# Performance work log

Hardware: AMD Instinct MI355X
Metric: run time of the kernel (lower is better)

The kernel has to match this reference:

```python
import jax, jax.numpy as jnp
import numpy as np

EPS = 1e-6
ALPHA = 0.2  # LeakyReLU negative slope


def layer_norm(x, g, b):
    mu = jnp.mean(x, axis=-1, keepdims=True)
    var = jnp.mean(jnp.square(x - mu), axis=-1, keepdims=True)
    return (x - mu) * jax.lax.rsqrt(var + EPS) * g + b


def graph_attention(x, bias, W, a_src, a_dst):
    # x: [B,N,D], bias: [B,N,N], W: [D, H*Dh], a_src/a_dst: [H, Dh]
    B, N, D = x.shape
    H, Dh = a_src.shape
    h = jnp.einsum('bnd,dhk->bhnk', x, W.reshape(D, H, Dh))  # [B,H,N,Dh]
    s = jnp.einsum('bhnk,hk->bhn', h, a_src)                 # source term
    t = jnp.einsum('bhnk,hk->bhn', h, a_dst)                 # target term
    e = jax.nn.leaky_relu(s[:, :, :, None] + t[:, :, None, :], ALPHA)
    e = e + bias[:, None, :, :]                              # graph mask/bias
    attn = jax.nn.softmax(e, axis=-1)                        # [B,H,N,N]
    out = jnp.einsum('bhij,bhjk->bhik', attn, h)             # [B,H,N,Dh]
    return out.transpose(0, 2, 1, 3).reshape(B, N, H * Dh)


def setup_inputs() -> dict:
    key = jax.random.key(0)
    ks = jax.random.split(key, 8)
    B, N, D, H = 2, 2048, 512, 8
    Dh = D // H
    sc = 1.0 / np.sqrt(D)
    return {
        'x': jax.random.normal(ks[0], (B, N, D), jnp.float32),
        'bias': jax.random.normal(ks[1], (B, N, N), jnp.float32),
        'W1': jax.random.normal(ks[2], (D, D), jnp.float32) * sc,
        'a_src1': jax.random.normal(ks[3], (H, Dh), jnp.float32) * sc,
        'a_dst1': jax.random.normal(ks[4], (H, Dh), jnp.float32) * sc,
        'g1': jnp.ones((D,), jnp.float32),
        'b1': jnp.zeros((D,), jnp.float32),
        'W2': jax.random.normal(ks[5], (D, D), jnp.float32) * sc,
        'a_src2': jax.random.normal(ks[6], (1, D), jnp.float32) * sc,
        'a_dst2': jax.random.normal(ks[7], (1, D), jnp.float32) * sc,
        'g2': jnp.ones((D,), jnp.float32),
        'b2': jnp.zeros((D,), jnp.float32),
    }


def reference(x, bias, W1, a_src1, a_dst1, g1, b1, W2, a_src2, a_dst2, g2, b2):
    # dropout is identity in eval mode
    attn_in = layer_norm(x, g1, b1)
    attn = graph_attention(attn_in, bias, W1, a_src1, a_dst1) + x
    attn_in2 = layer_norm(attn, g2, b2)
    out = graph_attention(attn_in2, bias, W2, a_src2, a_dst2) + attn
    return out
```

## Files before the change

kernel.cpp:

```cpp
#include <hip/hip_runtime.h>
#include <math.h>

#define NB 2
#define NN 2048
#define DD 512

typedef __attribute__((ext_vector_type(8))) short short8;
typedef __attribute__((ext_vector_type(4))) float f32x4;

__device__ __forceinline__ unsigned short f2bf(float x) {
  union { float f; unsigned u; } a;
  a.f = x;
  unsigned r = a.u + 0x7FFF + ((a.u >> 16) & 1);
  return (unsigned short)(r >> 16);
}
__device__ __forceinline__ float bf2f(unsigned short u) {
  union { unsigned u; float f; } a;
  a.u = ((unsigned)u) << 16;
  return a.f;
}
__device__ __forceinline__ unsigned cvtpk(float lo, float hi) {
  unsigned r;
  asm("v_cvt_pk_bf16_f32 %0, %1, %2" : "=v"(r) : "v"(lo), "v"(hi));
  return r;
}

__device__ __forceinline__ float waveReduceSum(float v) {
#pragma unroll
  for (int o = 32; o; o >>= 1) v += __shfl_down(v, o, 64);
  return v;
}
__device__ __forceinline__ float blockReduceSum(float v, float* red4) {
  int tid = threadIdx.x;
  __syncthreads();
  v = waveReduceSum(v);
  if ((tid & 63) == 0) red4[tid >> 6] = v;
  __syncthreads();
  return red4[0] + red4[1] + red4[2] + red4[3];
}

__global__ __launch_bounds__(256) void ln_kernel(const float* __restrict__ x,
                                                 const float* __restrict__ g,
                                                 const float* __restrict__ bb,
                                                 unsigned short* __restrict__ y) {
  int row = blockIdx.x;
  int t = threadIdx.x;
  const float* xr = x + (size_t)row * DD;
  __shared__ float red4[4];
  float2 v = *(const float2*)&xr[2 * t];
  float s = blockReduceSum(v.x + v.y, red4);
  float mu = s * (1.0f / 512.0f);
  float d0 = v.x - mu, d1 = v.y - mu;
  float ss = blockReduceSum(d0 * d0 + d1 * d1, red4);
  float rstd = rsqrtf(ss * (1.0f / 512.0f) + 1e-6f);
  float2 gg = *(const float2*)&g[2 * t];
  float2 bv = *(const float2*)&bb[2 * t];
  ushort2 o;
  o.x = f2bf(d0 * rstd * gg.x + bv.x);
  o.y = f2bf(d1 * rstd * gg.y + bv.y);
  *(ushort2*)&y[(size_t)row * DD + 2 * t] = o;
}

__global__ __launch_bounds__(256) void wt2_kernel(const float* __restrict__ W1,
                                                  const float* __restrict__ W2,
                                                  unsigned short* __restrict__ WT1,
                                                  unsigned short* __restrict__ WT2) {
  const float* W = blockIdx.z ? W2 : W1;
  unsigned short* WT = blockIdx.z ? WT2 : WT1;
  __shared__ float tile[64][65];
  int kt = blockIdx.x * 64, ct = blockIdx.y * 64;
  int t = threadIdx.x;
#pragma unroll
  for (int u = 0; u < 16; u++) {
    int lin = t + u * 256;
    int kl = lin >> 6, cl = lin & 63;
    tile[kl][cl] = W[(size_t)(kt + kl) * DD + ct + cl];
  }
  __syncthreads();
#pragma unroll
  for (int u = 0; u < 16; u++) {
    int lin = t + u * 256;
    int cl = lin >> 6, kl = lin & 63;
    WT[(size_t)(ct + cl) * DD + kt + kl] = f2bf(tile[kl][cl]);
  }
}

__global__ __launch_bounds__(256) void v2_kernel(
    const float* __restrict__ W1, const float* __restrict__ as1,
    const float* __restrict__ ad1, float* __restrict__ vs1, float* __restrict__ vd1,
    const float* __restrict__ W2, const float* __restrict__ as2,
    const float* __restrict__ ad2, float* __restrict__ vs2, float* __restrict__ vd2) {
  int slot = blockIdx.y;
  const float *W, *as, *ad;
  float *vs, *vd;
  int Dh, hoff;
  if (slot < 8) {
    W = W1; as = as1 + slot * 64; ad = ad1 + slot * 64;
    vs = vs1 + (size_t)slot * DD; vd = vd1 + (size_t)slot * DD;
    Dh = 64; hoff = slot * 64;
  } else {
    W = W2; as = as2; ad = ad2; vs = vs2; vd = vd2;
    Dh = 512; hoff = 0;
  }
  int t = threadIdx.x;
  int dl = t >> 2, kq = t & 3;
  int d = blockIdx.x * 64 + dl;
  int kn = Dh >> 2;
  const float* wr = W + (size_t)d * DD + hoff + kq * kn;
  const float* asp = as + kq * kn;
  const float* adp = ad + kq * kn;
  float s = 0.f, dd2 = 0.f;
  for (int k = 0; k < kn; k++) {
    float wv = wr[k];
    s += wv * asp[k];
    dd2 += wv * adp[k];
  }
  s += __shfl_xor(s, 1);
  s += __shfl_xor(s, 2);
  dd2 += __shfl_xor(dd2, 1);
  dd2 += __shfl_xor(dd2, 2);
  if (kq == 0) {
    vs[d] = s;
    vd[d] = dd2;
  }
}

__global__ __launch_bounds__(256) void biasH_kernel(const float* __restrict__ bias,
                                                    unsigned short* __restrict__ biasH) {
  int row = blockIdx.x;
  int t = threadIdx.x;
  const float* br = bias + (size_t)row * NN;
  float4 a = *(const float4*)&br[t * 4];
  float4 c = *(const float4*)&br[t * 4 + 1024];
  uint2 d0, d1;
  d0.x = cvtpk(a.x, a.y);
  d0.y = cvtpk(a.z, a.w);
  d1.x = cvtpk(c.x, c.y);
  d1.y = cvtpk(c.z, c.w);
  *(uint2*)&biasH[(size_t)row * NN + t * 4] = d0;
  *(uint2*)&biasH[(size_t)row * NN + t * 4 + 1024] = d1;
}

__global__ __launch_bounds__(256) void gemm_kernel(const unsigned short* __restrict__ A,
                                                   const unsigned short* __restrict__ BT,
                                                   unsigned short* __restrict__ hbT) {
  __shared__ float accL[4][16][65];
  int t = threadIdx.x, w = t >> 6, l = t & 63;
  int li = l & 15, lg = l >> 4;
  int R0 = blockIdx.x * 16;
  int c0 = blockIdx.y * 64;
  const unsigned short* ar = A + (size_t)(R0 + li) * DD + w * 128 + lg * 8;
  const unsigned short* br = BT + (size_t)(c0 + li) * DD + w * 128 + lg * 8;
  f32x4 acc[4] = {};
#pragma unroll
  for (int k0 = 0; k0 < 128; k0 += 32) {
    short8 af = *(const short8*)(ar + k0);
#pragma unroll
    for (int f = 0; f < 4; f++) {
      short8 bf = *(const short8*)(br + (size_t)f * 16 * DD + k0);
      acc[f] = __builtin_amdgcn_mfma_f32_16x16x32_bf16(af, bf, acc[f], 0, 0, 0);
    }
  }
#pragma unroll
  for (int f = 0; f < 4; f++)
#pragma unroll
    for (int r = 0; r < 4; r++) accL[w][lg * 4 + r][f * 16 + li] = acc[f][r];
  __syncthreads();
  int b = R0 >> 11, jT = (R0 & (NN - 1)) >> 4;
  int cT0 = c0 >> 4;
#pragma unroll
  for (int u = 0; u < 2; u++) {
    int idx = t + u * 256;
    int f = idx >> 7;
    int rem = idx & 127;
    int cl = rem >> 3, jlp = rem & 7;
    int cc = f * 16 + cl;
    float v0 = accL[0][2 * jlp][cc] + accL[1][2 * jlp][cc] + accL[2][2 * jlp][cc] +
               accL[3][2 * jlp][cc];
    float v1 = accL[0][2 * jlp + 1][cc] + accL[1][2 * jlp + 1][cc] +
               accL[2][2 * jlp + 1][cc] + accL[3][2 * jlp + 1][cc];
    size_t off = (((size_t)(b * (DD / 16) + cT0 + f) * (NN / 16)) + jT) * 256 +
                 cl * 16 + jlp * 2;
    *(unsigned*)(hbT + off) = cvtpk(v0, v1);
  }
}

__global__ __launch_bounds__(256) void st_kernel(const unsigned short* __restrict__ lnB,
                                                 const float* __restrict__ vs,
                                                 const float* __restrict__ vd,
                                                 float* __restrict__ sOut,
                                                 float* __restrict__ tOut, int HN) {
  int t = threadIdx.x, w = t >> 6, l = t & 63;
  int row = blockIdx.x * 4 + w;
  int b = row >> 11, n = row & (NN - 1);
  const unsigned short* lr = lnB + (size_t)row * DD + l * 8;
  union { short8 v; unsigned short u[8]; } xv;
  xv.v = *(const short8*)lr;
  float xf[8];
#pragma unroll
  for (int k = 0; k < 8; k++) xf[k] = bf2f(xv.u[k]);
  for (int h = 0; h < HN; h++) {
    const float* vsr = vs + (size_t)h * DD + l * 8;
    const float* vdr = vd + (size_t)h * DD + l * 8;
    float4 a0 = *(const float4*)vsr, a1 = *(const float4*)(vsr + 4);
    float4 c0 = *(const float4*)vdr, c1 = *(const float4*)(vdr + 4);
    float ps = xf[0] * a0.x + xf[1] * a0.y + xf[2] * a0.z + xf[3] * a0.w +
               xf[4] * a1.x + xf[5] * a1.y + xf[6] * a1.z + xf[7] * a1.w;
    float pd = xf[0] * c0.x + xf[1] * c0.y + xf[2] * c0.z + xf[3] * c0.w +
               xf[4] * c1.x + xf[5] * c1.y + xf[6] * c1.z + xf[7] * c1.w;
#pragma unroll
    for (int o = 32; o; o >>= 1) {
      ps += __shfl_xor(ps, o);
      pd += __shfl_xor(pd, o);
    }
    if (l == 0) {
      sOut[((size_t)b * HN + h) * NN + n] = ps;
      tOut[((size_t)b * HN + h) * NN + n] = pd;
    }
  }
}

template <int HN, int CCH>
__global__ __launch_bounds__(256) void pv_kernel(
    const unsigned short* __restrict__ hbT, const unsigned short* __restrict__ biasH,
    const float* __restrict__ sArr, const float* __restrict__ tArr,
    const float* __restrict__ res, float* __restrict__ out) {
  constexpr int DH = DD / HN;
  __shared__ unsigned short Pl[4][512];
  __shared__ float accL[4][16][33];
  __shared__ float sL[4][16];
  int t = threadIdx.x, w = t >> 6, l = t & 63;
  int li = l & 15, lg = l >> 4;
  int i0 = blockIdx.x * 16;
  int ck = blockIdx.y, bh = blockIdx.z;
  int h = bh % HN, b = bh / HN;
  int c0 = h * DH + ck * (CCH * 64);
  size_t bhN = (size_t)bh * NN;
  const float* trow = tArr + bhN;

  int rs = l >> 3;
  int js = (l & 7) * 4;
  int wq = (((l & 7) >> 1) ^ (rs & 3)) * 8 + (l & 1) * 4;
  float sv[2];
  sv[0] = sArr[bhN + i0 + rs];
  sv[1] = sArr[bhN + i0 + 8 + rs];
  const unsigned short* bbH = biasH + ((size_t)b * NN + i0) * NN;

  const unsigned short* vb =
      hbT + (((size_t)(b * (DD / 16) + (c0 >> 4)) * (NN / 16) + (lg >> 1)) * 256) +
      li * 16 + (lg & 1) * 8;
  int ra0 = li * 32 + ((lg ^ (li & 3)) * 8);

  const int jbeg = w * (NN / 4), jend = jbeg + NN / 4;
  f32x4 acc[CCH][4] = {};
  float psum[2] = {0.f, 0.f};

  float4 ptv = *(const float4*)&trow[jbeg + js];
  uint2 pb0 = *(const uint2*)&bbH[(size_t)(0 * 8 + rs) * NN + jbeg + js];
  uint2 pb1 = *(const uint2*)&bbH[(size_t)(1 * 8 + rs) * NN + jbeg + js];
  short8 nv[CCH][4];
#pragma unroll
  for (int cc = 0; cc < CCH; cc++)
#pragma unroll
    for (int f = 0; f < 4; f++)
      nv[cc][f] = *(const short8*)(vb + (size_t)jbeg * 16 + (size_t)(cc * 4 + f) * 32768);

  for (int jt = jbeg; jt < jend; jt += 32) {
    float4 tv = ptv;
    uint2 bq0 = pb0, bq1 = pb1;
    short8 v[CCH][4];
#pragma unroll
    for (int cc = 0; cc < CCH; cc++)
#pragma unroll
      for (int f = 0; f < 4; f++) v[cc][f] = nv[cc][f];
    if (jt + 32 < jend) {
      int jb = jt + 32 + js;
      ptv = *(const float4*)&trow[jb];
      pb0 = *(const uint2*)&bbH[(size_t)(0 * 8 + rs) * NN + jb];
      pb1 = *(const uint2*)&bbH[(size_t)(1 * 8 + rs) * NN + jb];
#pragma unroll
      for (int cc = 0; cc < CCH; cc++)
#pragma unroll
        for (int f = 0; f < 4; f++)
          nv[cc][f] = *(const short8*)(vb + (size_t)(jt + 32) * 16 +
                                       (size_t)(cc * 4 + f) * 32768);
    }
#pragma unroll
    for (int u = 0; u < 2; u++) {
      union { uint2 v; unsigned short q[4]; } bu;
      bu.v = u ? bq1 : bq0;
      int row = u * 8 + rs;
      float e0 = sv[u] + tv.x;
      float e1 = sv[u] + tv.y;
      float e2 = sv[u] + tv.z;
      float e3 = sv[u] + tv.w;
      e0 = fmaxf(e0, 0.2f * e0) + bf2f(bu.q[0]);
      e1 = fmaxf(e1, 0.2f * e1) + bf2f(bu.q[1]);
      e2 = fmaxf(e2, 0.2f * e2) + bf2f(bu.q[2]);
      e3 = fmaxf(e3, 0.2f * e3) + bf2f(bu.q[3]);
      float p0 = __expf(e0);
      float p1 = __expf(e1);
      float p2 = __expf(e2);
      float p3 = __expf(e3);
      psum[u] += (p0 + p1) + (p2 + p3);
      uint2 d;
      d.x = cvtpk(p0, p1);
      d.y = cvtpk(p2, p3);
      *(uint2*)&Pl[w][row * 32 + wq] = d;
    }
    short8 a0 = *(const short8*)&Pl[w][ra0];
    __builtin_amdgcn_s_setprio(1);
#pragma unroll
    for (int cc = 0; cc < CCH; cc++)
#pragma unroll
      for (int f = 0; f < 4; f++)
        acc[cc][f] = __builtin_amdgcn_mfma_f32_16x16x32_bf16(a0, v[cc][f], acc[cc][f], 0, 0, 0);
    __builtin_amdgcn_s_setprio(0);
  }
#pragma unroll
  for (int u = 0; u < 2; u++) {
    float r = psum[u];
    r += __shfl_xor(r, 1);
    r += __shfl_xor(r, 2);
    r += __shfl_xor(r, 4);
    if ((l & 7) == 0) sL[w][u * 8 + rs] = r;
  }
#pragma unroll
  for (int g = 0; g < 2 * CCH; g++) {
    int cc = g >> 1, half = g & 1;
#pragma unroll
    for (int f = 0; f < 2; f++)
#pragma unroll
      for (int r = 0; r < 4; r++)
        accL[w][lg * 4 + r][f * 16 + li] = acc[cc][half * 2 + f][r];
    __syncthreads();
    {
      int rr = t >> 4, cp = (t & 15) * 2;
      float S = sL[0][rr] + sL[1][rr] + sL[2][rr] + sL[3][rr];
      float inv = 1.0f / S;
      float2 O = {0.f, 0.f};
#pragma unroll
      for (int w2 = 0; w2 < 4; w2++) {
        O.x += accL[w2][rr][cp];
        O.y += accL[w2][rr][cp + 1];
      }
      size_t ix = ((size_t)b * NN + i0 + rr) * DD + c0 + cc * 64 + half * 32 + cp;
      float2 rv = *(const float2*)&res[ix];
      float2 ov = {O.x * inv + rv.x, O.y * inv + rv.y};
      *(float2*)&out[ix] = ov;
    }
    __syncthreads();
  }
}

extern "C" void kernel_launch(void* const* d_in, const int* in_sizes, int n_in,
                              void* d_out, int out_size, void* d_ws, size_t ws_size,
                              hipStream_t stream) {
  const float* x = (const float*)d_in[0];
  const float* bias = (const float*)d_in[1];
  const float* W1 = (const float*)d_in[2];
  const float* asrc1 = (const float*)d_in[3];
  const float* adst1 = (const float*)d_in[4];
  const float* g1 = (const float*)d_in[5];
  const float* b1 = (const float*)d_in[6];
  const float* W2 = (const float*)d_in[7];
  const float* asrc2 = (const float*)d_in[8];
  const float* adst2 = (const float*)d_in[9];
  const float* g2 = (const float*)d_in[10];
  const float* b2 = (const float*)d_in[11];
  float* out = (float*)d_out;
  float* ws = (float*)d_ws;

  const size_t RC = (size_t)NB * NN * DD;
  float* attnBuf = ws;
  unsigned short* lnB = (unsigned short*)(ws + RC);
  unsigned short* hbT = (unsigned short*)(ws + RC + RC / 2);
  unsigned short* WT1 = (unsigned short*)(ws + 2 * RC);
  unsigned short* WT2 = WT1 + (size_t)DD * DD;
  float* vs1 = (float*)(WT2 + (size_t)DD * DD);
  float* vd1 = vs1 + 8 * DD;
  float* vs2 = vd1 + 8 * DD;
  float* vd2 = vs2 + DD;
  float* sBuf = vd2 + DD;
  float* tBuf = sBuf + 16 * NN;
  unsigned short* biasH = (unsigned short*)(tBuf + 16 * NN);

  const int rows = NB * NN;

  hipLaunchKernelGGL(wt2_kernel, dim3(8, 8, 2), dim3(256), 0, stream, W1, W2, WT1, WT2);
  hipLaunchKernelGGL(v2_kernel, dim3(8, 9), dim3(256), 0, stream, W1, asrc1, adst1, vs1, vd1,
                     W2, asrc2, adst2, vs2, vd2);
  hipLaunchKernelGGL(biasH_kernel, dim3(rows), dim3(256), 0, stream, bias, biasH);

  hipLaunchKernelGGL(ln_kernel, dim3(rows), dim3(256), 0, stream, x, g1, b1, lnB);
  hipLaunchKernelGGL(gemm_kernel, dim3(256, 8), dim3(256), 0, stream, lnB, WT1, hbT);
  hipLaunchKernelGGL(st_kernel, dim3(rows / 4), dim3(256), 0, stream, lnB, vs1, vd1, sBuf, tBuf, 8);
  hipLaunchKernelGGL((pv_kernel<8, 1>), dim3(128, 1, 16), dim3(256), 0, stream, hbT, biasH,
                     sBuf, tBuf, x, attnBuf);

  hipLaunchKernelGGL(ln_kernel, dim3(rows), dim3(256), 0, stream, attnBuf, g2, b2, lnB);
  hipLaunchKernelGGL(gemm_kernel, dim3(256, 8), dim3(256), 0, stream, lnB, WT2, hbT);
  hipLaunchKernelGGL(st_kernel, dim3(rows / 4), dim3(256), 0, stream, lnB, vs2, vd2, sBuf, tBuf, 1);
  hipLaunchKernelGGL((pv_kernel<1, 2>), dim3(128, 4, 2), dim3(256), 0, stream, hbT, biasH,
                     sBuf, tBuf, attnBuf, out);
}
```

Before: 170.5 us.

## Retile transposed V layout into 64-column blocks and compute softmax row sums via MFMA

The projection kernel now writes the transposed bf16 h in 64-column blocks, so the four 16-column fragments a PV block reads for one key tile sit next to each other rather than 32K elements apart. This is meant to improve locality and DRAM page behaviour on the V loads. The PV kernel also drops the per-lane fp32 running sums and shuffle reduction, and computes the softmax denominator with one extra MFMA against a vector of bf16 ones. The denominator is therefore summed from bf16-rounded probabilities, which matches the numerator but costs one more MFMA per tile.

New measurement: 167.2 us. About the same (-1.9%).

```diff
diff --git a/kernel.cpp b/kernel.cpp
--- a/kernel.cpp
+++ b/kernel.cpp
@@ -167,7 +167,6 @@
     for (int r = 0; r < 4; r++) accL[w][lg * 4 + r][f * 16 + li] = acc[f][r];
   __syncthreads();
   int b = R0 >> 11, jT = (R0 & (NN - 1)) >> 4;
-  int cT0 = c0 >> 4;
 #pragma unroll
   for (int u = 0; u < 2; u++) {
     int idx = t + u * 256;
@@ -179,8 +178,8 @@
                accL[3][2 * jlp][cc];
     float v1 = accL[0][2 * jlp + 1][cc] + accL[1][2 * jlp + 1][cc] +
                accL[2][2 * jlp + 1][cc] + accL[3][2 * jlp + 1][cc];
-    size_t off = (((size_t)(b * (DD / 16) + cT0 + f) * (NN / 16)) + jT) * 256 +
-                 cl * 16 + jlp * 2;
+    size_t off = (((size_t)(b * (DD / 64) + blockIdx.y) * (NN / 16)) + jT) * 1024 +
+                 f * 256 + cl * 16 + jlp * 2;
     *(unsigned*)(hbT + off) = cvtpk(v0, v1);
   }
 }
@@ -228,7 +227,7 @@
   constexpr int DH = DD / HN;
   __shared__ unsigned short Pl[4][512];
   __shared__ float accL[4][16][33];
-  __shared__ float sL[4][16];
+  __shared__ float sLa[4][16];
   int t = threadIdx.x, w = t >> 6, l = t & 63;
   int li = l & 15, lg = l >> 4;
   int i0 = blockIdx.x * 16;
@@ -244,30 +243,36 @@
   float sv[2];
   sv[0] = sArr[bhN + i0 + rs];
   sv[1] = sArr[bhN + i0 + 8 + rs];
-  const unsigned short* bbH = biasH + ((size_t)b * NN + i0) * NN;
-
-  const unsigned short* vb =
-      hbT + (((size_t)(b * (DD / 16) + (c0 >> 4)) * (NN / 16) + (lg >> 1)) * 256) +
-      li * 16 + (lg & 1) * 8;
+  const unsigned short* bb0 = biasH + ((size_t)b * NN + i0 + rs) * NN;
+  const unsigned short* bb1 = bb0 + (size_t)8 * NN;
+
+  const unsigned short* vbase =
+      hbT + ((size_t)(b * (DD / 64) + (c0 >> 6)) * (NN / 16)) * 1024 +
+      (lg >> 1) * 1024 + li * 16 + (lg & 1) * 8;
   int ra0 = li * 32 + ((lg ^ (li & 3)) * 8);
+
+  union { short8 v; unsigned short q[8]; } ones;
+#pragma unroll
+  for (int k = 0; k < 8; k++) ones.q[k] = 0x3F80;
 
   const int jbeg = w * (NN / 4), jend = jbeg + NN / 4;
   f32x4 acc[CCH][4] = {};
-  float psum[2] = {0.f, 0.f};
+  f32x4 accS = {0.f, 0.f, 0.f, 0.f};
 
   float4 ptv = *(const float4*)&trow[jbeg + js];
-  uint2 pb0 = *(const uint2*)&bbH[(size_t)(0 * 8 + rs) * NN + jbeg + js];
-  uint2 pb1 = *(const uint2*)&bbH[(size_t)(1 * 8 + rs) * NN + jbeg + js];
+  uint2 pq0 = *(const uint2*)&bb0[jbeg + js];
+  uint2 pq1 = *(const uint2*)&bb1[jbeg + js];
   short8 nv[CCH][4];
 #pragma unroll
-  for (int cc = 0; cc < CCH; cc++)
-#pragma unroll
-    for (int f = 0; f < 4; f++)
-      nv[cc][f] = *(const short8*)(vb + (size_t)jbeg * 16 + (size_t)(cc * 4 + f) * 32768);
+  for (int cc = 0; cc < CCH; cc++) {
+    const unsigned short* vp = vbase + (size_t)cc * ((NN / 16) * 1024) + (size_t)jbeg * 64;
+#pragma unroll
+    for (int f = 0; f < 4; f++) nv[cc][f] = *(const short8*)(vp + f * 256);
+  }
 
   for (int jt = jbeg; jt < jend; jt += 32) {
     float4 tv = ptv;
-    uint2 bq0 = pb0, bq1 = pb1;
+    uint2 bq0 = pq0, bq1 = pq1;
     short8 v[CCH][4];
 #pragma unroll
     for (int cc = 0; cc < CCH; cc++)
@@ -276,14 +281,15 @@
     if (jt + 32 < jend) {
       int jb = jt + 32 + js;
       ptv = *(const float4*)&trow[jb];
-      pb0 = *(const uint2*)&bbH[(size_t)(0 * 8 + rs) * NN + jb];
-      pb1 = *(const uint2*)&bbH[(size_t)(1 * 8 + rs) * NN + jb];
-#pragma unroll
-      for (int cc = 0; cc < CCH; cc++)
-#pragma unroll
-        for (int f = 0; f < 4; f++)
-          nv[cc][f] = *(const short8*)(vb + (size_t)(jt + 32) * 16 +
-                                       (size_t)(cc * 4 + f) * 32768);
+      pq0 = *(const uint2*)&bb0[jb];
+      pq1 = *(const uint2*)&bb1[jb];
+#pragma unroll
+      for (int cc = 0; cc < CCH; cc++) {
+        const unsigned short* vp =
+            vbase + (size_t)cc * ((NN / 16) * 1024) + (size_t)(jt + 32) * 64;
+#pragma unroll
+        for (int f = 0; f < 4; f++) nv[cc][f] = *(const short8*)(vp + f * 256);
+      }
     }
 #pragma unroll
     for (int u = 0; u < 2; u++) {
@@ -298,18 +304,14 @@
       e1 = fmaxf(e1, 0.2f * e1) + bf2f(bu.q[1]);
       e2 = fmaxf(e2, 0.2f * e2) + bf2f(bu.q[2]);
       e3 = fmaxf(e3, 0.2f * e3) + bf2f(bu.q[3]);
-      float p0 = __expf(e0);
-      float p1 = __expf(e1);
-      float p2 = __expf(e2);
-      float p3 = __expf(e3);
-      psum[u] += (p0 + p1) + (p2 + p3);
       uint2 d;
-      d.x = cvtpk(p0, p1);
-      d.y = cvtpk(p2, p3);
+      d.x = cvtpk(__expf(e0), __expf(e1));
+      d.y = cvtpk(__expf(e2), __expf(e3));
       *(uint2*)&Pl[w][row * 32 + wq] = d;
     }
     short8 a0 = *(const short8*)&Pl[w][ra0];
     __builtin_amdgcn_s_setprio(1);
+    accS = __builtin_amdgcn_mfma_f32_16x16x32_bf16(a0, ones.v, accS, 0, 0, 0);
 #pragma unroll
     for (int cc = 0; cc < CCH; cc++)
 #pragma unroll
@@ -317,13 +319,9 @@
         acc[cc][f] = __builtin_amdgcn_mfma_f32_16x16x32_bf16(a0, v[cc][f], acc[cc][f], 0, 0, 0);
     __builtin_amdgcn_s_setprio(0);
   }
-#pragma unroll
-  for (int u = 0; u < 2; u++) {
-    float r = psum[u];
-    r += __shfl_xor(r, 1);
-    r += __shfl_xor(r, 2);
-    r += __shfl_xor(r, 4);
-    if ((l & 7) == 0) sL[w][u * 8 + rs] = r;
+  if (li == 0) {
+#pragma unroll
+    for (int r = 0; r < 4; r++) sLa[w][lg * 4 + r] = accS[r];
   }
 #pragma unroll
   for (int g = 0; g < 2 * CCH; g++) {
@@ -336,7 +334,7 @@
     __syncthreads();
     {
       int rr = t >> 4, cp = (t & 15) * 2;
-      float S = sL[0][rr] + sL[1][rr] + sL[2][rr] + sL[3][rr];
+      float S = sLa[0][rr] + sLa[1][rr] + sLa[2][rr] + sLa[3][rr];
       float inv = 1.0f / S;
       float2 O = {0.f, 0.f};
 #pragma unroll
```
